# Performance work log

Measured on AMD Instinct MI355X. Metric: run time of the kernel, lower is better.

Reference implementation:

```python
import jax, jax.numpy as jnp
import numpy as np

B, T, C, H, R = 2, 2048, 2048, 16, 8
D = C // H  # head_dim = 128


def _rope_cache(seq_len, dim, theta=10000.0):
    pos = jnp.arange(seq_len, dtype=jnp.float32)[:, None]            # [T,1]
    idx = jnp.arange(0, dim, 2, dtype=jnp.float32)                   # [D/2]
    freqs = 1.0 / (theta ** (idx / dim))
    ang = pos * freqs                                                # [T, D/2]
    return jnp.cos(ang), jnp.sin(ang)


def setup_inputs() -> dict:
    key = jax.random.key(0)
    ks = jax.random.split(key, 16)
    s = 0.02
    inp = {"x": jax.random.normal(ks[0], (B, T, C), dtype=jnp.float32)}
    i = 1
    for nm in ("q", "k", "v", "p"):
        inp[f"{nm}_w"] = jax.random.normal(ks[i], (C, C), dtype=jnp.float32) * s; i += 1
        inp[f"{nm}_b"] = jnp.zeros((C,), dtype=jnp.float32)
        inp[f"{nm}_A"] = jax.random.normal(ks[i], (C, R), dtype=jnp.float32) * s; i += 1
        inp[f"{nm}_B"] = jax.random.normal(ks[i], (R, C), dtype=jnp.float32) * s; i += 1
    cos, sin = _rope_cache(T, D)
    inp["cos"] = cos
    inp["sin"] = sin
    inp["mask"] = jnp.tril(jnp.ones((T, T), dtype=bool))  # causal SDPA mask
    inp["use_lora"] = 1
    return inp


def _lora_linear(x, w, b, A, Bm, use_lora):
    # base GEMM + bias, plus low-rank adapter x @ A @ B (intended path)
    out = x @ w.T + b
    if use_lora:
        out = out + (x @ A) @ Bm
    return out


def _apply_rope(x, cos, sin):
    # x: [B,H,T,D]; cos/sin: [T, D/2] broadcast over batch & heads
    x1 = x[..., ::2]
    x2 = x[..., 1::2]
    y = jnp.stack((x1 * cos - x2 * sin, x1 * sin + x2 * cos), axis=-1)
    return y.reshape(x.shape)


def reference(x, q_w, q_b, q_A, q_B, k_w, k_b, k_A, k_B,
              v_w, v_b, v_A, v_B, p_w, p_b, p_A, p_B,
              cos, sin, mask, use_lora):
    Bsz, Tl, Cd = x.shape
    q = _lora_linear(x, q_w, q_b, q_A, q_B, use_lora).reshape(Bsz, Tl, H, D).transpose(0, 2, 1, 3)
    k = _lora_linear(x, k_w, k_b, k_A, k_B, use_lora).reshape(Bsz, Tl, H, D).transpose(0, 2, 1, 3)
    v = _lora_linear(x, v_w, v_b, v_A, v_B, use_lora).reshape(Bsz, Tl, H, D).transpose(0, 2, 1, 3)
    q = _apply_rope(q, cos, sin)
    k = _apply_rope(k, cos, sin)
    # scaled dot-product attention with boolean mask (True = attend)
    scale = 1.0 / jnp.sqrt(jnp.asarray(D, dtype=x.dtype))
    scores = jnp.einsum('bhqd,bhkd->bhqk', q, k) * scale          # [B,H,T,T]
    neg = jnp.asarray(jnp.finfo(scores.dtype).min, dtype=scores.dtype)
    scores = jnp.where(mask, scores, neg)
    attn = jax.nn.softmax(scores, axis=-1)
    out = jnp.einsum('bhqk,bhkd->bhqd', attn, v)                  # [B,H,T,D]
    y = out.transpose(0, 2, 1, 3).reshape(Bsz, Tl, Cd)
    return _lora_linear(y, p_w, p_b, p_A, p_B, use_lora)
```

## Files before the change

kernel.cpp:

```cpp
#include <hip/hip_runtime.h>

typedef _Float16 f16;
typedef _Float16 f16x4 __attribute__((ext_vector_type(4)));
typedef _Float16 f16x8 __attribute__((ext_vector_type(8)));
typedef __fp16 hf2 __attribute__((ext_vector_type(2)));
typedef float f32x4 __attribute__((ext_vector_type(4)));

#define DEV static __device__ __forceinline__

DEV void gl_lds16(const void* g, void* l) {
  __builtin_amdgcn_global_load_lds(
      (const __attribute__((address_space(1))) void*)g,
      (__attribute__((address_space(3))) void*)l, 16, 0, 0);
}

DEV uint pkrtz(float a, float b) {
  hf2 h = __builtin_amdgcn_cvt_pkrtz(a, b);
  return __builtin_bit_cast(uint, h);
}

__global__ void cast_f16_kernel(const float* __restrict__ x,
                                const float* __restrict__ w0,
                                const float* __restrict__ w1,
                                const float* __restrict__ w2,
                                const float* __restrict__ w3,
                                f16* __restrict__ xb, f16* __restrict__ b0,
                                f16* __restrict__ b1, f16* __restrict__ b2,
                                f16* __restrict__ b3) {
  const int total4 = (8388608 + 4 * 4194304) / 4;
  for (int i = blockIdx.x * blockDim.x + threadIdx.x; i < total4;
       i += gridDim.x * blockDim.x) {
    int e = i << 2;
    const float* s; f16* d; int off;
    if (e < 8388608)        { s = x;  d = xb; off = e; }
    else if (e < 12582912)  { s = w0; d = b0; off = e - 8388608; }
    else if (e < 16777216)  { s = w1; d = b1; off = e - 12582912; }
    else if (e < 20971520)  { s = w2; d = b2; off = e - 16777216; }
    else                    { s = w3; d = b3; off = e - 20971520; }
    float4 v = *(const float4*)(s + off);
    f16x4 hv = {(f16)v.x, (f16)v.y, (f16)v.z, (f16)v.w};
    *(f16x4*)(d + off) = hv;
  }
}

__global__ __launch_bounds__(256) void lora_x_kernel(
    const float* __restrict__ x, const float* __restrict__ Aq,
    const float* __restrict__ Ak, const float* __restrict__ Av,
    float* __restrict__ la) {
  const int wave = threadIdx.x >> 6, lane = threadIdx.x & 63;
  const int m = blockIdx.x * 4 + wave;
  const float* xrow = x + (size_t)m * 2048;
  const float* As[3] = {Aq, Ak, Av};
  float acc[3][8] = {};
  for (int i = 0; i < 32; ++i) {
    int k = i * 64 + lane;
    float xv = xrow[k];
#pragma unroll
    for (int nm = 0; nm < 3; ++nm) {
      const float4* ap = (const float4*)(As[nm] + (size_t)k * 8);
      float4 a0 = ap[0], a1 = ap[1];
      acc[nm][0] += xv * a0.x; acc[nm][1] += xv * a0.y;
      acc[nm][2] += xv * a0.z; acc[nm][3] += xv * a0.w;
      acc[nm][4] += xv * a1.x; acc[nm][5] += xv * a1.y;
      acc[nm][6] += xv * a1.z; acc[nm][7] += xv * a1.w;
    }
  }
#pragma unroll
  for (int nm = 0; nm < 3; ++nm)
#pragma unroll
    for (int r = 0; r < 8; ++r) {
      float v = acc[nm][r];
#pragma unroll
      for (int off = 1; off < 64; off <<= 1) v += __shfl_xor(v, off);
      acc[nm][r] = v;
    }
  if (lane == 0) {
#pragma unroll
    for (int nm = 0; nm < 3; ++nm)
#pragma unroll
      for (int r = 0; r < 8; ++r)
        la[nm * 32768 + (size_t)m * 8 + r] = acc[nm][r];
  }
}

__global__ __launch_bounds__(256) void lora_p_kernel(
    const f16* __restrict__ y, const float* __restrict__ Ap,
    float* __restrict__ lap) {
  const int wave = threadIdx.x >> 6, lane = threadIdx.x & 63;
  const int m = blockIdx.x * 4 + wave;
  const f16* yrow = y + (size_t)m * 2048;
  float acc[8] = {};
  for (int i = 0; i < 4; ++i) {
    int k0 = i * 512 + lane * 8;
    f16x8 yv = *(const f16x8*)(yrow + k0);
#pragma unroll
    for (int j = 0; j < 8; ++j) {
      float xv = (float)yv[j];
      const float4* ap = (const float4*)(Ap + (size_t)(k0 + j) * 8);
      float4 a0 = ap[0], a1 = ap[1];
      acc[0] += xv * a0.x; acc[1] += xv * a0.y;
      acc[2] += xv * a0.z; acc[3] += xv * a0.w;
      acc[4] += xv * a1.x; acc[5] += xv * a1.y;
      acc[6] += xv * a1.z; acc[7] += xv * a1.w;
    }
  }
#pragma unroll
  for (int r = 0; r < 8; ++r) {
    float v = acc[r];
#pragma unroll
    for (int off = 1; off < 64; off <<= 1) v += __shfl_xor(v, off);
    acc[r] = v;
  }
  if (lane == 0) {
#pragma unroll
    for (int r = 0; r < 8; ++r) lap[(size_t)m * 8 + r] = acc[r];
  }
}

template <int MODE>
__global__ __launch_bounds__(256, 2) void gemm_kernel(
    const f16* __restrict__ A, const f16* __restrict__ Bw,
    const float* __restrict__ bias, const float* __restrict__ la,
    const float* __restrict__ Bm, const int* __restrict__ use_lora,
    const float* __restrict__ cosT, const float* __restrict__ sinT,
    void* __restrict__ out) {
  __shared__ char smem[32768];
  const int tid = threadIdx.x;
  const int wave = tid >> 6, lane = tid & 63;
  const int lr = lane & 15, lg = lane >> 4;
  const int bm = blockIdx.x >> 4, bn = blockIdx.x & 15;
  const int m0 = bm << 7, n0 = bn << 7;
  const int wr = wave >> 1, wc = wave & 1;

  uint aoff[4], boff[4];
#pragma unroll
  for (int r = 0; r < 4; ++r) {
    uint beta = (uint)(wave * 4 + r) * 1024 + (uint)lane * 16;
    uint row = beta >> 7;
    uint c = (beta & 127u) ^ ((row & 7u) << 4);
    aoff[r] = (uint)(m0 + row) * 4096 + c;
    boff[r] = (uint)(n0 + row) * 4096 + c;
  }
  const char* Ab = (const char*)A;
  const char* Bb = (const char*)Bw;

  f32x4 acc[4][4] = {};

  for (int kt = 0; kt < 32; ++kt) {
    __syncthreads();
    const int kb = kt << 7;
#pragma unroll
    for (int r = 0; r < 4; ++r) {
      gl_lds16(Ab + (size_t)(aoff[r] + kb), smem + (wave * 4 + r) * 1024);
      gl_lds16(Bb + (size_t)(boff[r] + kb), smem + 16384 + (wave * 4 + r) * 1024);
    }
    __syncthreads();

    f16x8 af[2][4], bf[2][4];
#pragma unroll
    for (int ks = 0; ks < 2; ++ks) {
#pragma unroll
      for (int mi = 0; mi < 4; ++mi) {
        int row = wr * 64 + mi * 16 + lr;
        int c = (ks * 64 + lg * 16) ^ ((row & 7) << 4);
        af[ks][mi] = *(const f16x8*)(smem + row * 128 + c);
      }
#pragma unroll
      for (int ni = 0; ni < 4; ++ni) {
        int row = wc * 64 + ni * 16 + lr;
        int c = (ks * 64 + lg * 16) ^ ((row & 7) << 4);
        bf[ks][ni] = *(const f16x8*)(smem + 16384 + row * 128 + c);
      }
    }
    __builtin_amdgcn_s_setprio(1);
#pragma unroll
    for (int ks = 0; ks < 2; ++ks)
#pragma unroll
      for (int mi = 0; mi < 4; ++mi)
#pragma unroll
        for (int ni = 0; ni < 4; ++ni)
          acc[mi][ni] = __builtin_amdgcn_mfma_f32_16x16x32_f16(
              af[ks][mi], bf[ks][ni], acc[mi][ni], 0, 0, 0);
    __builtin_amdgcn_s_setprio(0);
  }

  const int ul = use_lora[0];
  __syncthreads();

  float bv[4], bml[4][8];
#pragma unroll
  for (int ni = 0; ni < 4; ++ni) {
    int n = n0 + wc * 64 + ni * 16 + lr;
    bv[ni] = bias[n];
    if (ul) {
#pragma unroll
      for (int r = 0; r < 8; ++r) bml[ni][r] = Bm[r * 2048 + n];
    }
  }

  f16* stg = (f16*)smem;
#pragma unroll
  for (int mi = 0; mi < 4; ++mi) {
    const int mbase = m0 + wr * 64 + mi * 16 + lg * 4;
    float lar[4][8];
    if (ul) {
#pragma unroll
      for (int rg = 0; rg < 4; ++rg) {
        const float4* lp = (const float4*)(la + (size_t)(mbase + rg) * 8);
        float4 l0 = lp[0], l1 = lp[1];
        lar[rg][0] = l0.x; lar[rg][1] = l0.y; lar[rg][2] = l0.z; lar[rg][3] = l0.w;
        lar[rg][4] = l1.x; lar[rg][5] = l1.y; lar[rg][6] = l1.z; lar[rg][7] = l1.w;
      }
    }
#pragma unroll
    for (int ni = 0; ni < 4; ++ni) {
      const int n = n0 + wc * 64 + ni * 16 + lr;
#pragma unroll
      for (int rg = 0; rg < 4; ++rg) {
        float v = acc[mi][ni][rg] + bv[ni];
        if (ul) {
#pragma unroll
          for (int r = 0; r < 8; ++r) v += lar[rg][r] * bml[ni][r];
        }
        if (MODE == 0) {
          float pv = __shfl_xor(v, 1);
          const int m = mbase + rg;
          const int t = m & 2047;
          const int d = n & 127;
          const int ci = t * 64 + (d >> 1);
          float cs = cosT[ci], sn = sinT[ci];
          float res = ((lane & 1) == 0) ? (v * cs - pv * sn)
                                        : (pv * sn + v * cs);
          stg[(wr * 64 + mi * 16 + lg * 4 + rg) * 128 +
              (wc * 64 + ni * 16 + lr)] = (f16)res;
        } else if (MODE == 1) {
          stg[(wr * 64 + mi * 16 + lg * 4 + rg) * 128 +
              (wc * 64 + ni * 16 + lr)] = (f16)v;
        } else {
          ((float*)out)[(size_t)(mbase + rg) * 2048 + n] = v;
        }
      }
    }
  }

  if (MODE < 2) {
    __syncthreads();
    if (MODE == 0) {
      const long b_ = m0 >> 11;
      const int tb = m0 & 2047;
      char* obase = (char*)out + ((b_ * 16 + bn) * 2048 + tb) * 256;
#pragma unroll
      for (int p = 0; p < 8; ++p) {
        int s = p * 4096 + tid * 16;
        int row = s >> 8, c = s & 255;
        *(uint4*)(obase + (long)row * 256 + c) = *(const uint4*)(smem + s);
      }
    } else {
      char* obase = (char*)out + ((long)m0 * 2048 + n0) * 2;
#pragma unroll
      for (int p = 0; p < 8; ++p) {
        int s = p * 4096 + tid * 16;
        int row = s >> 8, c = s & 255;
        *(uint4*)(obase + (long)row * 4096 + c) = *(const uint4*)(smem + s);
      }
    }
  }
}

__global__ void transpose_v_kernel(const ushort* __restrict__ vbi,
                                   ushort* __restrict__ vto) {
  __shared__ ushort tile[32][33];
  const int t0 = blockIdx.x << 5;
  const int d0 = blockIdx.y << 5;
  const int bh = blockIdx.z;
  const int b = bh >> 4, h = bh & 15;
  const int tx = threadIdx.x, ty = threadIdx.y;
  const ushort* src = vbi + ((size_t)(b * 2048 + t0)) * 2048 + h * 128 + d0;
#pragma unroll
  for (int i = 0; i < 4; ++i)
    tile[ty + 8 * i][tx] = src[(size_t)(ty + 8 * i) * 2048 + tx];
  __syncthreads();
  ushort* dst = vto + ((size_t)bh * 128 + d0) * 2048 + t0;
#pragma unroll
  for (int i = 0; i < 4; ++i)
    dst[(size_t)(ty + 8 * i) * 2048 + tx] = tile[tx][ty + 8 * i];
}

__global__ __launch_bounds__(256, 2) void attn_kernel(
    const f16* __restrict__ qr, const f16* __restrict__ kr,
    const f16* __restrict__ vt, f16* __restrict__ y) {
  extern __shared__ char smem[];
  const int tid = threadIdx.x, wave = tid >> 6, lane = tid & 63;
  const int lr = lane & 15, lg = lane >> 4;
  const int qt = 15 - (int)blockIdx.x;
  const int q0 = qt << 7;
  const int h = blockIdx.y, b = blockIdx.z;
  const long bh = b * 16 + h;
  const int nt = 2 * qt + 2;

  const char* kbase = (const char*)kr + bh * 2048 * 256;
  const char* vbase = (const char*)vt + bh * 128 * 4096;

  f16x8 qf[2][4];
#pragma unroll
  for (int g = 0; g < 2; ++g) {
    const char* qb =
        (const char*)qr + (bh * 2048 + q0 + wave * 32 + g * 16 + lr) * 256;
#pragma unroll
    for (int ks = 0; ks < 4; ++ks)
      qf[g][ks] = *(const f16x8*)(qb + ks * 64 + lg * 16);
  }

  f32x4 o[2][8] = {};
  float mrow[2] = {-3e38f, -3e38f};
  float lsum[2] = {0.f, 0.f};
  const float SC2 = 0.12752551286084103f;

  auto STAGE = [&](int kv0, int bsel) {
    char* Ks = smem + bsel * 32768;
    char* Vs = Ks + 16384;
#pragma unroll
    for (int r = 0; r < 4; ++r) {
      uint s = (uint)(wave * 4 + r) * 1024 + (uint)lane * 16;
      uint rowk = s >> 8, ck = (s & 255u) ^ ((rowk & 7u) << 4);
      gl_lds16(kbase + (size_t)(kv0 + rowk) * 256 + ck,
               Ks + (wave * 4 + r) * 1024);
      uint rowv = s >> 7, cv = (s & 127u) ^ ((rowv & 7u) << 4);
      gl_lds16(vbase + (size_t)rowv * 4096 + kv0 * 2 + cv,
               Vs + (wave * 4 + r) * 1024);
    }
  };

  STAGE(0, 0);
  __syncthreads();

  for (int kt = 0; kt < nt; ++kt) {
    const int kv0 = kt << 6;
    if (kt + 1 < nt) STAGE((kt + 1) << 6, (kt + 1) & 1);
    const char* Ks = smem + (kt & 1) * 32768;
    const char* Vs = Ks + 16384;

    if (kv0 <= q0 + wave * 32 + 31) {
      f32x4 sa[2][4] = {};
      __builtin_amdgcn_s_setprio(1);
#pragma unroll
      for (int ks = 0; ks < 4; ++ks)
#pragma unroll
        for (int n = 0; n < 4; ++n) {
          int row = n * 16 + lr;
          int c = (ks * 64 + lg * 16) ^ ((row & 7) << 4);
          f16x8 kf = *(const f16x8*)(Ks + row * 256 + c);
          sa[0][n] =
              __builtin_amdgcn_mfma_f32_16x16x32_f16(kf, qf[0][ks], sa[0][n], 0, 0, 0);
          sa[1][n] =
              __builtin_amdgcn_mfma_f32_16x16x32_f16(kf, qf[1][ks], sa[1][n], 0, 0, 0);
        }
      __builtin_amdgcn_s_setprio(0);

      f16x8 pf[2][2];
#pragma unroll
      for (int g = 0; g < 2; ++g) {
        const int qgbase = q0 + wave * 32 + g * 16;
        float L[16];
        float pm = -3e38f;
        const bool dm = (kv0 + 63 > qgbase);
#pragma unroll
        for (int n = 0; n < 4; ++n)
#pragma unroll
          for (int rg = 0; rg < 4; ++rg) {
            float Lv = sa[g][n][rg] * SC2;
            if (dm && (kv0 + n * 16 + lg * 4 + rg > qgbase + lr)) Lv = -3e37f;
            L[n * 4 + rg] = Lv;
            pm = fmaxf(pm, Lv);
          }
        pm = fmaxf(pm, __shfl_xor(pm, 16));
        pm = fmaxf(pm, __shfl_xor(pm, 32));
        float mn = fmaxf(mrow[g], pm);
        float alpha = exp2f(mrow[g] - mn);
        mrow[g] = mn;
        float ps = 0.f;
#pragma unroll
        for (int i = 0; i < 16; ++i) {
          float p = exp2f(L[i] - mn);
          L[i] = p;
          ps += p;
        }
        ps += __shfl_xor(ps, 16);
        ps += __shfl_xor(ps, 32);
        lsum[g] = lsum[g] * alpha + ps;
#pragma unroll
        for (int dt = 0; dt < 8; ++dt)
#pragma unroll
          for (int rg = 0; rg < 4; ++rg) o[g][dt][rg] *= alpha;

#pragma unroll
        for (int ks2 = 0; ks2 < 2; ++ks2) {
          uint w0 = pkrtz(L[8 * ks2 + 0], L[8 * ks2 + 1]);
          uint w1 = pkrtz(L[8 * ks2 + 2], L[8 * ks2 + 3]);
          uint w2 = pkrtz(L[8 * ks2 + 4], L[8 * ks2 + 5]);
          uint w3 = pkrtz(L[8 * ks2 + 6], L[8 * ks2 + 7]);
          int src1 = ((lg & 1) << 5) + lr;
          int src2 = src1 + 16;
          uint a0 = __shfl((int)w0, src1), a1 = __shfl((int)w1, src1);
          uint a2 = __shfl((int)w2, src1), a3 = __shfl((int)w3, src1);
          uint b0 = __shfl((int)w0, src2), b1 = __shfl((int)w1, src2);
          uint b2 = __shfl((int)w2, src2), b3 = __shfl((int)w3, src2);
          const bool hi = (lg >> 1) != 0;
          uint4 uu;
          uu.x = hi ? a2 : a0;
          uu.y = hi ? a3 : a1;
          uu.z = hi ? b2 : b0;
          uu.w = hi ? b3 : b1;
          pf[g][ks2] = __builtin_bit_cast(f16x8, uu);
        }
      }

#pragma unroll
      for (int ks2 = 0; ks2 < 2; ++ks2) {
        __builtin_amdgcn_s_setprio(1);
#pragma unroll
        for (int dt = 0; dt < 8; ++dt) {
          int drow = dt * 16 + lr;
          int c = (ks2 * 64 + lg * 16) ^ ((drow & 7) << 4);
          f16x8 vf = *(const f16x8*)(Vs + drow * 128 + c);
          o[0][dt] =
              __builtin_amdgcn_mfma_f32_16x16x32_f16(vf, pf[0][ks2], o[0][dt], 0, 0, 0);
          o[1][dt] =
              __builtin_amdgcn_mfma_f32_16x16x32_f16(vf, pf[1][ks2], o[1][dt], 0, 0, 0);
        }
        __builtin_amdgcn_s_setprio(0);
      }
    }
    __syncthreads();
  }

#pragma unroll
  for (int g = 0; g < 2; ++g) {
    const float inv = 1.f / lsum[g];
    const int row = wave * 32 + g * 16 + lr;
#pragma unroll
    for (int dt = 0; dt < 8; ++dt) {
      uint lo = pkrtz(o[g][dt][0] * inv, o[g][dt][1] * inv);
      uint hi2 = pkrtz(o[g][dt][2] * inv, o[g][dt][3] * inv);
      int c = (dt * 32 + lg * 8) ^ ((row & 7) << 4);
      uint2 w;
      w.x = lo;
      w.y = hi2;
      *(uint2*)(smem + row * 256 + c) = w;
    }
  }
  __syncthreads();
#pragma unroll
  for (int p = 0; p < 8; ++p) {
    int s = p * 4096 + tid * 16;
    int row = s >> 8, cb = s & 255;
    int c = cb ^ ((row & 7) << 4);
    char* dst =
        (char*)y + ((long)(b * 2048 + q0 + row) * 2048 + h * 128) * 2 + cb;
    *(uint4*)dst = *(const uint4*)(smem + row * 256 + c);
  }
}

extern "C" void kernel_launch(void* const* d_in, const int* in_sizes, int n_in,
                              void* d_out, int out_size, void* d_ws,
                              size_t ws_size, hipStream_t stream) {
  (void)in_sizes; (void)n_in; (void)out_size; (void)ws_size;
  const float* x   = (const float*)d_in[0];
  const float* q_w = (const float*)d_in[1];
  const float* q_b = (const float*)d_in[2];
  const float* q_A = (const float*)d_in[3];
  const float* q_B = (const float*)d_in[4];
  const float* k_w = (const float*)d_in[5];
  const float* k_b = (const float*)d_in[6];
  const float* k_A = (const float*)d_in[7];
  const float* k_B = (const float*)d_in[8];
  const float* v_w = (const float*)d_in[9];
  const float* v_b = (const float*)d_in[10];
  const float* v_A = (const float*)d_in[11];
  const float* v_B = (const float*)d_in[12];
  const float* p_w = (const float*)d_in[13];
  const float* p_b = (const float*)d_in[14];
  const float* p_A = (const float*)d_in[15];
  const float* p_B = (const float*)d_in[16];
  const float* cosT = (const float*)d_in[17];
  const float* sinT = (const float*)d_in[18];
  const int* use_lora = (const int*)d_in[20];

  char* ws = (char*)d_ws;
  f16* xb  = (f16*)(ws);
  f16* wqb = (f16*)(ws + 16777216);
  f16* wkb = (f16*)(ws + 25165824);
  f16* wvb = (f16*)(ws + 33554432);
  f16* wpb = (f16*)(ws + 41943040);
  float* la = (float*)(ws + 50331648);
  f16* qr  = (f16*)(ws + 50855936);
  f16* kr  = (f16*)(ws + 67633152);
  f16* vb  = (f16*)(ws + 84410368);
  f16* vt  = (f16*)(ws);
  f16* y   = vb;
  float* lap = la + 98304;

  cast_f16_kernel<<<dim3(2048), dim3(256), 0, stream>>>(
      x, q_w, k_w, v_w, p_w, xb, wqb, wkb, wvb, wpb);
  lora_x_kernel<<<dim3(1024), dim3(256), 0, stream>>>(x, q_A, k_A, v_A, la);
  gemm_kernel<0><<<dim3(512), dim3(256), 0, stream>>>(
      xb, wqb, q_b, la, q_B, use_lora, cosT, sinT, (void*)qr);
  gemm_kernel<0><<<dim3(512), dim3(256), 0, stream>>>(
      xb, wkb, k_b, la + 32768, k_B, use_lora, cosT, sinT, (void*)kr);
  gemm_kernel<1><<<dim3(512), dim3(256), 0, stream>>>(
      xb, wvb, v_b, la + 65536, v_B, use_lora, nullptr, nullptr, (void*)vb);
  transpose_v_kernel<<<dim3(64, 4, 32), dim3(32, 8), 0, stream>>>(
      (const ushort*)vb, (ushort*)vt);
  attn_kernel<<<dim3(16, 16, 2), dim3(256), 65536, stream>>>(qr, kr, vt, y);
  lora_p_kernel<<<dim3(1024), dim3(256), 0, stream>>>(y, p_A, lap);
  gemm_kernel<2><<<dim3(512), dim3(256), 0, stream>>>(
      y, wpb, p_b, lap, p_B, use_lora, nullptr, nullptr, d_out);
}
```

Measured before the change: 393.4 us.

## Fuse QKV GEMMs into one launch, double-buffer GEMM loads, fuse V transpose and x cast

Replaces the three separate Q/K/V GEMM launches with a single grid-z launch driven by a per-slice argument struct. The GEMM main loop now double-buffers its LDS tiles to overlap global loads with MFMA work. The V transpose is done in the GEMM epilogue, the x cast moves into the LoRA-x kernel, and the softmax scale is folded into Q. Attention also hoists its staging offsets, uses tree reductions, and skips the running-max rescale unless the max grows past a threshold. Together these remove launches, extra passes over memory and per-tile rescale work, at the cost of 64KB of LDS per GEMM block and runtime mode branches.

```diff
diff --git a/kernel.cpp b/kernel.cpp
--- a/kernel.cpp
+++ b/kernel.cpp
@@ -19,24 +19,27 @@
   return __builtin_bit_cast(uint, h);
 }
 
-__global__ void cast_f16_kernel(const float* __restrict__ x,
-                                const float* __restrict__ w0,
-                                const float* __restrict__ w1,
-                                const float* __restrict__ w2,
-                                const float* __restrict__ w3,
-                                f16* __restrict__ xb, f16* __restrict__ b0,
-                                f16* __restrict__ b1, f16* __restrict__ b2,
-                                f16* __restrict__ b3) {
-  const int total4 = (8388608 + 4 * 4194304) / 4;
+DEV f32x4 MFMA(f16x8 a, f16x8 b, f32x4 c) {
+  return __builtin_amdgcn_mfma_f32_16x16x32_f16(a, b, c, 0, 0, 0);
+}
+
+#define SC2Q 0.12752551286084103f
+
+__global__ void cast_w_kernel(const float* __restrict__ w0,
+                              const float* __restrict__ w1,
+                              const float* __restrict__ w2,
+                              const float* __restrict__ w3,
+                              f16* __restrict__ b0, f16* __restrict__ b1,
+                              f16* __restrict__ b2, f16* __restrict__ b3) {
+  const int total4 = 4 * 4194304 / 4;
   for (int i = blockIdx.x * blockDim.x + threadIdx.x; i < total4;
        i += gridDim.x * blockDim.x) {
     int e = i << 2;
     const float* s; f16* d; int off;
-    if (e < 8388608)        { s = x;  d = xb; off = e; }
-    else if (e < 12582912)  { s = w0; d = b0; off = e - 8388608; }
-    else if (e < 16777216)  { s = w1; d = b1; off = e - 12582912; }
-    else if (e < 20971520)  { s = w2; d = b2; off = e - 16777216; }
-    else                    { s = w3; d = b3; off = e - 20971520; }
+    if (e < 4194304)        { s = w0; d = b0; off = e; }
+    else if (e < 8388608)   { s = w1; d = b1; off = e - 4194304; }
+    else if (e < 12582912)  { s = w2; d = b2; off = e - 8388608; }
+    else                    { s = w3; d = b3; off = e - 12582912; }
     float4 v = *(const float4*)(s + off);
     f16x4 hv = {(f16)v.x, (f16)v.y, (f16)v.z, (f16)v.w};
     *(f16x4*)(d + off) = hv;
@@ -46,15 +49,17 @@
 __global__ __launch_bounds__(256) void lora_x_kernel(
     const float* __restrict__ x, const float* __restrict__ Aq,
     const float* __restrict__ Ak, const float* __restrict__ Av,
-    float* __restrict__ la) {
+    float* __restrict__ la, f16* __restrict__ xb) {
   const int wave = threadIdx.x >> 6, lane = threadIdx.x & 63;
   const int m = blockIdx.x * 4 + wave;
   const float* xrow = x + (size_t)m * 2048;
+  f16* xbrow = xb + (size_t)m * 2048;
   const float* As[3] = {Aq, Ak, Av};
   float acc[3][8] = {};
   for (int i = 0; i < 32; ++i) {
     int k = i * 64 + lane;
     float xv = xrow[k];
+    xbrow[k] = (f16)xv;
 #pragma unroll
     for (int nm = 0; nm < 3; ++nm) {
       const float4* ap = (const float4*)(As[nm] + (size_t)k * 8);
@@ -117,20 +122,38 @@
   }
 }
 
-template <int MODE>
-__global__ __launch_bounds__(256, 2) void gemm_kernel(
-    const f16* __restrict__ A, const f16* __restrict__ Bw,
-    const float* __restrict__ bias, const float* __restrict__ la,
-    const float* __restrict__ Bm, const int* __restrict__ use_lora,
-    const float* __restrict__ cosT, const float* __restrict__ sinT,
-    void* __restrict__ out) {
-  __shared__ char smem[32768];
+struct GemmArgs {
+  const f16* A;
+  const f16* W[3];
+  const float* bias[3];
+  const float* la[3];
+  const float* Bm[3];
+  void* out[3];
+  int mode[3];
+};
+
+__global__ __launch_bounds__(256, 2) void gemm2_kernel(
+    GemmArgs args, const int* __restrict__ use_lora,
+    const float* __restrict__ cosT, const float* __restrict__ sinT) {
+  extern __shared__ char smem[];
+  const int z = blockIdx.y;
+  const f16* A = args.A;
+  const f16* Bw = args.W[z];
+  const float* bias = args.bias[z];
+  const float* la = args.la[z];
+  const float* Bm = args.Bm[z];
+  void* out = args.out[z];
+  const int mode = args.mode[z];
+
   const int tid = threadIdx.x;
   const int wave = tid >> 6, lane = tid & 63;
   const int lr = lane & 15, lg = lane >> 4;
-  const int bm = blockIdx.x >> 4, bn = blockIdx.x & 15;
+  const int bm = (int)blockIdx.x >> 4, bn = (int)blockIdx.x & 15;
   const int m0 = bm << 7, n0 = bn << 7;
   const int wr = wave >> 1, wc = wave & 1;
+
+  const char* Ab = (const char*)A;
+  const char* Bb = (const char*)Bw;
 
   uint aoff[4], boff[4];
 #pragma unroll
@@ -141,21 +164,27 @@
     aoff[r] = (uint)(m0 + row) * 4096 + c;
     boff[r] = (uint)(n0 + row) * 4096 + c;
   }
-  const char* Ab = (const char*)A;
-  const char* Bb = (const char*)Bw;
+
+  auto STAGE = [&](int kt, int b) {
+    char* dst = smem + b * 32768;
+    const size_t kb = (size_t)kt << 7;
+#pragma unroll
+    for (int r = 0; r < 4; ++r) {
+      gl_lds16(Ab + (aoff[r] + kb), dst + (wave * 4 + r) * 1024);
+      gl_lds16(Bb + (boff[r] + kb), dst + 16384 + (wave * 4 + r) * 1024);
+    }
+  };
 
   f32x4 acc[4][4] = {};
 
+  STAGE(0, 0);
   for (int kt = 0; kt < 32; ++kt) {
-    __syncthreads();
-    const int kb = kt << 7;
-#pragma unroll
-    for (int r = 0; r < 4; ++r) {
-      gl_lds16(Ab + (size_t)(aoff[r] + kb), smem + (wave * 4 + r) * 1024);
-      gl_lds16(Bb + (size_t)(boff[r] + kb), smem + 16384 + (wave * 4 + r) * 1024);
-    }
-    __syncthreads();
-
+    const int b = kt & 1;
+    asm volatile("s_waitcnt vmcnt(0) lgkmcnt(0)" ::: "memory");
+    __builtin_amdgcn_s_barrier();
+    if (kt + 1 < 32) STAGE(kt + 1, b ^ 1);
+
+    const char* buf = smem + b * 32768;
     f16x8 af[2][4], bf[2][4];
 #pragma unroll
     for (int ks = 0; ks < 2; ++ks) {
@@ -163,13 +192,13 @@
       for (int mi = 0; mi < 4; ++mi) {
         int row = wr * 64 + mi * 16 + lr;
         int c = (ks * 64 + lg * 16) ^ ((row & 7) << 4);
-        af[ks][mi] = *(const f16x8*)(smem + row * 128 + c);
+        af[ks][mi] = *(const f16x8*)(buf + row * 128 + c);
       }
 #pragma unroll
       for (int ni = 0; ni < 4; ++ni) {
         int row = wc * 64 + ni * 16 + lr;
         int c = (ks * 64 + lg * 16) ^ ((row & 7) << 4);
-        bf[ks][ni] = *(const f16x8*)(smem + 16384 + row * 128 + c);
+        bf[ks][ni] = *(const f16x8*)(buf + 16384 + row * 128 + c);
       }
     }
     __builtin_amdgcn_s_setprio(1);
@@ -179,13 +208,13 @@
       for (int mi = 0; mi < 4; ++mi)
 #pragma unroll
         for (int ni = 0; ni < 4; ++ni)
-          acc[mi][ni] = __builtin_amdgcn_mfma_f32_16x16x32_f16(
-              af[ks][mi], bf[ks][ni], acc[mi][ni], 0, 0, 0);
+          acc[mi][ni] = MFMA(af[ks][mi], bf[ks][ni], acc[mi][ni]);
     __builtin_amdgcn_s_setprio(0);
   }
 
   const int ul = use_lora[0];
-  __syncthreads();
+  asm volatile("s_waitcnt lgkmcnt(0)" ::: "memory");
+  __builtin_amdgcn_s_barrier();
 
   float bv[4], bml[4][8];
 #pragma unroll
@@ -198,7 +227,6 @@
     }
   }
 
-  f16* stg = (f16*)smem;
 #pragma unroll
   for (int mi = 0; mi < 4; ++mi) {
     const int mbase = m0 + wr * 64 + mi * 16 + lg * 4;
@@ -222,20 +250,19 @@
 #pragma unroll
           for (int r = 0; r < 8; ++r) v += lar[rg][r] * bml[ni][r];
         }
-        if (MODE == 0) {
+        const int mm = wr * 64 + mi * 16 + lg * 4 + rg;
+        const int nn = wc * 64 + ni * 16 + lr;
+        if (mode <= 1) {
           float pv = __shfl_xor(v, 1);
-          const int m = mbase + rg;
-          const int t = m & 2047;
-          const int d = n & 127;
-          const int ci = t * 64 + (d >> 1);
+          const int t = (mbase + rg) & 2047;
+          const int ci = t * 64 + ((n & 127) >> 1);
           float cs = cosT[ci], sn = sinT[ci];
           float res = ((lane & 1) == 0) ? (v * cs - pv * sn)
                                         : (pv * sn + v * cs);
-          stg[(wr * 64 + mi * 16 + lg * 4 + rg) * 128 +
-              (wc * 64 + ni * 16 + lr)] = (f16)res;
-        } else if (MODE == 1) {
-          stg[(wr * 64 + mi * 16 + lg * 4 + rg) * 128 +
-              (wc * 64 + ni * 16 + lr)] = (f16)v;
+          if (mode == 0) res *= SC2Q;
+          ((f16*)smem)[mm * 128 + nn] = (f16)res;
+        } else if (mode == 2) {
+          *(f16*)(smem + nn * 256 + ((mm * 2) ^ ((nn & 7) << 4))) = (f16)v;
         } else {
           ((float*)out)[(size_t)(mbase + rg) * 2048 + n] = v;
         }
@@ -243,47 +270,31 @@
     }
   }
 
-  if (MODE < 2) {
-    __syncthreads();
-    if (MODE == 0) {
-      const long b_ = m0 >> 11;
-      const int tb = m0 & 2047;
-      char* obase = (char*)out + ((b_ * 16 + bn) * 2048 + tb) * 256;
-#pragma unroll
-      for (int p = 0; p < 8; ++p) {
-        int s = p * 4096 + tid * 16;
-        int row = s >> 8, c = s & 255;
-        *(uint4*)(obase + (long)row * 256 + c) = *(const uint4*)(smem + s);
-      }
-    } else {
-      char* obase = (char*)out + ((long)m0 * 2048 + n0) * 2;
-#pragma unroll
-      for (int p = 0; p < 8; ++p) {
-        int s = p * 4096 + tid * 16;
-        int row = s >> 8, c = s & 255;
-        *(uint4*)(obase + (long)row * 4096 + c) = *(const uint4*)(smem + s);
-      }
-    }
-  }
-}
-
-__global__ void transpose_v_kernel(const ushort* __restrict__ vbi,
-                                   ushort* __restrict__ vto) {
-  __shared__ ushort tile[32][33];
-  const int t0 = blockIdx.x << 5;
-  const int d0 = blockIdx.y << 5;
-  const int bh = blockIdx.z;
-  const int b = bh >> 4, h = bh & 15;
-  const int tx = threadIdx.x, ty = threadIdx.y;
-  const ushort* src = vbi + ((size_t)(b * 2048 + t0)) * 2048 + h * 128 + d0;
-#pragma unroll
-  for (int i = 0; i < 4; ++i)
-    tile[ty + 8 * i][tx] = src[(size_t)(ty + 8 * i) * 2048 + tx];
-  __syncthreads();
-  ushort* dst = vto + ((size_t)bh * 128 + d0) * 2048 + t0;
-#pragma unroll
-  for (int i = 0; i < 4; ++i)
-    dst[(size_t)(ty + 8 * i) * 2048 + tx] = tile[tx][ty + 8 * i];
+  if (mode <= 1) {
+    __builtin_amdgcn_s_barrier();
+    const long b_ = m0 >> 11;
+    const int tb = m0 & 2047;
+    char* obase = (char*)out + ((b_ * 16 + bn) * 2048 + tb) * 256;
+#pragma unroll
+    for (int p = 0; p < 8; ++p) {
+      int s = p * 4096 + tid * 16;
+      int row = s >> 8, c = s & 255;
+      *(uint4*)(obase + (long)row * 256 + c) = *(const uint4*)(smem + s);
+    }
+  } else if (mode == 2) {
+    __builtin_amdgcn_s_barrier();
+    const long b_ = m0 >> 11;
+    const int tb = m0 & 2047;
+    char* obase = (char*)out + (((b_ * 16 + bn) * 128) * 2048 + tb) * 2;
+#pragma unroll
+    for (int p = 0; p < 8; ++p) {
+      int s = p * 4096 + tid * 16;
+      int row = s >> 8, cb = s & 255;
+      int c = cb ^ ((row & 7) << 4);
+      uint4 val = *(const uint4*)(smem + row * 256 + c);
+      *(uint4*)(obase + (long)row * 4096 + cb) = val;
+    }
+  }
 }
 
 __global__ __launch_bounds__(256, 2) void attn_kernel(
@@ -301,6 +312,16 @@
   const char* kbase = (const char*)kr + bh * 2048 * 256;
   const char* vbase = (const char*)vt + bh * 128 * 4096;
 
+  uint koff[4], voff[4];
+#pragma unroll
+  for (int r = 0; r < 4; ++r) {
+    uint s = (uint)(wave * 4 + r) * 1024 + (uint)lane * 16;
+    uint rowk = s >> 8;
+    koff[r] = rowk * 256 + ((s & 255u) ^ ((rowk & 7u) << 4));
+    uint rowv = s >> 7;
+    voff[r] = rowv * 4096 + ((s & 127u) ^ ((rowv & 7u) << 4));
+  }
+
   f16x8 qf[2][4];
 #pragma unroll
   for (int g = 0; g < 2; ++g) {
@@ -314,20 +335,14 @@
   f32x4 o[2][8] = {};
   float mrow[2] = {-3e38f, -3e38f};
   float lsum[2] = {0.f, 0.f};
-  const float SC2 = 0.12752551286084103f;
 
   auto STAGE = [&](int kv0, int bsel) {
     char* Ks = smem + bsel * 32768;
     char* Vs = Ks + 16384;
 #pragma unroll
     for (int r = 0; r < 4; ++r) {
-      uint s = (uint)(wave * 4 + r) * 1024 + (uint)lane * 16;
-      uint rowk = s >> 8, ck = (s & 255u) ^ ((rowk & 7u) << 4);
-      gl_lds16(kbase + (size_t)(kv0 + rowk) * 256 + ck,
-               Ks + (wave * 4 + r) * 1024);
-      uint rowv = s >> 7, cv = (s & 127u) ^ ((rowv & 7u) << 4);
-      gl_lds16(vbase + (size_t)rowv * 4096 + kv0 * 2 + cv,
-               Vs + (wave * 4 + r) * 1024);
+      gl_lds16(kbase + (size_t)kv0 * 256 + koff[r], Ks + (wave * 4 + r) * 1024);
+      gl_lds16(vbase + (size_t)kv0 * 2 + voff[r], Vs + (wave * 4 + r) * 1024);
     }
   };
 
@@ -350,10 +365,8 @@
           int row = n * 16 + lr;
           int c = (ks * 64 + lg * 16) ^ ((row & 7) << 4);
           f16x8 kf = *(const f16x8*)(Ks + row * 256 + c);
-          sa[0][n] =
-              __builtin_amdgcn_mfma_f32_16x16x32_f16(kf, qf[0][ks], sa[0][n], 0, 0, 0);
-          sa[1][n] =
-              __builtin_amdgcn_mfma_f32_16x16x32_f16(kf, qf[1][ks], sa[1][n], 0, 0, 0);
+          sa[0][n] = MFMA(kf, qf[0][ks], sa[0][n]);
+          sa[1][n] = MFMA(kf, qf[1][ks], sa[1][n]);
         }
       __builtin_amdgcn_s_setprio(0);
 
@@ -362,36 +375,45 @@
       for (int g = 0; g < 2; ++g) {
         const int qgbase = q0 + wave * 32 + g * 16;
         float L[16];
-        float pm = -3e38f;
         const bool dm = (kv0 + 63 > qgbase);
 #pragma unroll
         for (int n = 0; n < 4; ++n)
 #pragma unroll
           for (int rg = 0; rg < 4; ++rg) {
-            float Lv = sa[g][n][rg] * SC2;
+            float Lv = sa[g][n][rg];
             if (dm && (kv0 + n * 16 + lg * 4 + rg > qgbase + lr)) Lv = -3e37f;
             L[n * 4 + rg] = Lv;
-            pm = fmaxf(pm, Lv);
           }
-        pm = fmaxf(pm, __shfl_xor(pm, 16));
-        pm = fmaxf(pm, __shfl_xor(pm, 32));
-        float mn = fmaxf(mrow[g], pm);
-        float alpha = exp2f(mrow[g] - mn);
-        mrow[g] = mn;
-        float ps = 0.f;
-#pragma unroll
-        for (int i = 0; i < 16; ++i) {
-          float p = exp2f(L[i] - mn);
-          L[i] = p;
-          ps += p;
+        float m0a = fmaxf(L[0], L[1]),  m1a = fmaxf(L[2], L[3]);
+        float m2a = fmaxf(L[4], L[5]),  m3a = fmaxf(L[6], L[7]);
+        float m4a = fmaxf(L[8], L[9]),  m5a = fmaxf(L[10], L[11]);
+        float m6a = fmaxf(L[12], L[13]), m7a = fmaxf(L[14], L[15]);
+        float m0b = fmaxf(m0a, m1a), m1b = fmaxf(m2a, m3a);
+        float m2b = fmaxf(m4a, m5a), m3b = fmaxf(m6a, m7a);
+        float pm = fmaxf(fmaxf(m0b, m1b), fmaxf(m2b, m3b));
+        if (!__all(pm <= mrow[g] + 8.f)) {
+          pm = fmaxf(pm, __shfl_xor(pm, 16));
+          pm = fmaxf(pm, __shfl_xor(pm, 32));
+          float mn = fmaxf(mrow[g], pm);
+          float alpha = exp2f(mrow[g] - mn);
+          mrow[g] = mn;
+          lsum[g] *= alpha;
+#pragma unroll
+          for (int dt = 0; dt < 8; ++dt)
+#pragma unroll
+            for (int rg = 0; rg < 4; ++rg) o[g][dt][rg] *= alpha;
         }
+        const float mn = mrow[g];
+#pragma unroll
+        for (int i = 0; i < 16; ++i) L[i] = exp2f(L[i] - mn);
+        float s0 = L[0] + L[1], s1 = L[2] + L[3], s2 = L[4] + L[5],
+              s3 = L[6] + L[7], s4 = L[8] + L[9], s5 = L[10] + L[11],
+              s6 = L[12] + L[13], s7 = L[14] + L[15];
+        float t0 = s0 + s1, t1 = s2 + s3, t2 = s4 + s5, t3 = s6 + s7;
+        float ps = (t0 + t1) + (t2 + t3);
         ps += __shfl_xor(ps, 16);
         ps += __shfl_xor(ps, 32);
-        lsum[g] = lsum[g] * alpha + ps;
-#pragma unroll
-        for (int dt = 0; dt < 8; ++dt)
-#pragma unroll
-          for (int rg = 0; rg < 4; ++rg) o[g][dt][rg] *= alpha;
+        lsum[g] += ps;
 
 #pragma unroll
         for (int ks2 = 0; ks2 < 2; ++ks2) {
@@ -423,10 +445,8 @@
           int drow = dt * 16 + lr;
           int c = (ks2 * 64 + lg * 16) ^ ((drow & 7) << 4);
           f16x8 vf = *(const f16x8*)(Vs + drow * 128 + c);
-          o[0][dt] =
-              __builtin_amdgcn_mfma_f32_16x16x32_f16(vf, pf[0][ks2], o[0][dt], 0, 0, 0);
-          o[1][dt] =
-              __builtin_amdgcn_mfma_f32_16x16x32_f16(vf, pf[1][ks2], o[1][dt], 0, 0, 0);
+          o[0][dt] = MFMA(vf, pf[0][ks2], o[0][dt]);
+          o[1][dt] = MFMA(vf, pf[1][ks2], o[1][dt]);
         }
         __builtin_amdgcn_s_setprio(0);
       }
@@ -495,24 +515,36 @@
   float* la = (float*)(ws + 50331648);
   f16* qr  = (f16*)(ws + 50855936);
   f16* kr  = (f16*)(ws + 67633152);
-  f16* vb  = (f16*)(ws + 84410368);
-  f16* vt  = (f16*)(ws);
-  f16* y   = vb;
+  f16* vt  = (f16*)(ws + 84410368);
+  f16* y   = xb;
   float* lap = la + 98304;
 
-  cast_f16_kernel<<<dim3(2048), dim3(256), 0, stream>>>(
-      x, q_w, k_w, v_w, p_w, xb, wqb, wkb, wvb, wpb);
-  lora_x_kernel<<<dim3(1024), dim3(256), 0, stream>>>(x, q_A, k_A, v_A, la);
-  gemm_kernel<0><<<dim3(512), dim3(256), 0, stream>>>(
-      xb, wqb, q_b, la, q_B, use_lora, cosT, sinT, (void*)qr);
-  gemm_kernel<0><<<dim3(512), dim3(256), 0, stream>>>(
-      xb, wkb, k_b, la + 32768, k_B, use_lora, cosT, sinT, (void*)kr);
-  gemm_kernel<1><<<dim3(512), dim3(256), 0, stream>>>(
-      xb, wvb, v_b, la + 65536, v_B, use_lora, nullptr, nullptr, (void*)vb);
-  transpose_v_kernel<<<dim3(64, 4, 32), dim3(32, 8), 0, stream>>>(
-      (const ushort*)vb, (ushort*)vt);
+  cast_w_kernel<<<dim3(2048), dim3(256), 0, stream>>>(
+      q_w, k_w, v_w, p_w, wqb, wkb, wvb, wpb);
+  lora_x_kernel<<<dim3(1024), dim3(256), 0, stream>>>(x, q_A, k_A, v_A, la, xb);
+
+  GemmArgs qkv;
+  qkv.A = xb;
+  qkv.W[0] = wqb;  qkv.W[1] = wkb;  qkv.W[2] = wvb;
+  qkv.bias[0] = q_b; qkv.bias[1] = k_b; qkv.bias[2] = v_b;
+  qkv.la[0] = la; qkv.la[1] = la + 32768; qkv.la[2] = la + 65536;
+  qkv.Bm[0] = q_B; qkv.Bm[1] = k_B; qkv.Bm[2] = v_B;
+  qkv.out[0] = qr; qkv.out[1] = kr; qkv.out[2] = vt;
+  qkv.mode[0] = 0; qkv.mode[1] = 1; qkv.mode[2] = 2;
+  gemm2_kernel<<<dim3(512, 3), dim3(256), 65536, stream>>>(
+      qkv, use_lora, cosT, sinT);
+
   attn_kernel<<<dim3(16, 16, 2), dim3(256), 65536, stream>>>(qr, kr, vt, y);
   lora_p_kernel<<<dim3(1024), dim3(256), 0, stream>>>(y, p_A, lap);
-  gemm_kernel<2><<<dim3(512), dim3(256), 0, stream>>>(
-      y, wpb, p_b, lap, p_B, use_lora, nullptr, nullptr, d_out);
-}
+
+  GemmArgs pp;
+  pp.A = y;
+  pp.W[0] = wpb;  pp.W[1] = wpb;  pp.W[2] = wpb;
+  pp.bias[0] = p_b; pp.bias[1] = p_b; pp.bias[2] = p_b;
+  pp.la[0] = lap; pp.la[1] = lap; pp.la[2] = lap;
+  pp.Bm[0] = p_B; pp.Bm[1] = p_B; pp.Bm[2] = p_B;
+  pp.out[0] = d_out; pp.out[1] = d_out; pp.out[2] = d_out;
+  pp.mode[0] = 3; pp.mode[1] = 3; pp.mode[2] = 3;
+  gemm2_kernel<<<dim3(512, 1), dim3(256), 65536, stream>>>(
+      pp, use_lora, nullptr, nullptr);
+}
```

Result: faster. 369.6 us (-6.0%).
